# Performance work log

Measured on AMD Instinct MI355X. Metric: run time of the kernel, lower is better.

Reference implementation:

```python
import jax, jax.numpy as jnp
import numpy as np

LEN = 2048

def setup_inputs() -> dict:
    key = jax.random.key(0)
    k1, k2 = jax.random.split(key)
    x = jax.random.normal(k1, (LEN,), dtype=jnp.float32)
    y = jax.random.normal(k2, (LEN,), dtype=jnp.float32)
    return {"x": x, "y": y}

def reference(x, y):
    # Classic DTW DP with squared-difference cost.
    # Original torch code clamps indices with max(i-1,0)/max(j-1,0); because
    # DTW[i,j] is still +inf when read, the clamped reads reduce to the
    # standard recurrence: row 0 is a cumulative sum, col 0 uses only 'up',
    # interior uses min(up, left, diag).
    inf = jnp.float32(jnp.inf)
    cost0 = (x[0] - y) ** 2            # [len2]
    row0 = jnp.cumsum(cost0)           # DTW row i=0

    def row_step(prev_row, xi):
        cost = (xi - y) ** 2                                   # [len2]
        diag = jnp.concatenate([prev_row[:1], prev_row[:-1]])  # prev_row[j-1], clamped at j=0
        def cell(left, cud):
            c, up, dg = cud
            v = c + jnp.minimum(jnp.minimum(up, left), dg)
            return v, v
        # left init = inf => at j=0 min reduces to min(up, diag) = prev_row[0]
        _, new_row = jax.lax.scan(cell, inf, (cost, prev_row, diag))
        return new_row, None

    last_row, _ = jax.lax.scan(row_step, row0, x[1:])
    return jnp.sqrt(last_row[-1])
```

## Files before the change

### kernel.cpp

```cpp
#include <hip/hip_runtime.h>
#include <math.h>


#define NLEN   2048
#define NW     4
#define CSTEP  64
#define SPB    (CSTEP / 2)
#define DSKEW  192
#define PAD    128
#define RROW   (PAD + 2176)
#define YPAD   128
#define TAUMAX 2112
#define GTOT   (TAUMAX + (NW - 1) * DSKEW + CSTEP)
#define INFV   1e30f

typedef float f32x2 __attribute__((ext_vector_type(2)));

__device__ __forceinline__ float dpp_shr1(float v, float inj) {
    int r = __builtin_amdgcn_update_dpp(
        __builtin_bit_cast(int, inj), __builtin_bit_cast(int, v),
        0x138 , 0xF, 0xF, false );
    return __builtin_bit_cast(float, r);
}
__device__ __forceinline__ float rdlane(float v, int l) {
    return __builtin_bit_cast(float,
        __builtin_amdgcn_readlane(__builtin_bit_cast(int, v), l));
}
__device__ __forceinline__ float min3f(float a, float b, float c) {
    unsigned ia = __builtin_bit_cast(unsigned, a);
    unsigned ib = __builtin_bit_cast(unsigned, b);
    unsigned ic = __builtin_bit_cast(unsigned, c);
    unsigned m  = __builtin_elementwise_min(
                      __builtin_elementwise_min(ia, ib), ic);
    return __builtin_bit_cast(float, m);
}

__global__ __launch_bounds__(256, 1) void dtw_kernel(const float* __restrict__ X,
                                                     const float* __restrict__ Y,
                                                     float* __restrict__ out) {
    __shared__ __align__(16) float yB[YPAD + NLEN + YPAD];
    __shared__ float ring[(NW + 1) * RROW];
    float* yS = yB + YPAD;

    const int tid  = threadIdx.x;
    const int w    = tid >> 6;
    const int lane = tid & 63;

    {
        const float4* Y4 = (const float4*)Y;
        float4* y4 = (float4*)(yB + YPAD);
        y4[tid]       = Y4[tid];
        y4[tid + 256] = Y4[tid + 256];
        if (tid < YPAD) {
            yB[tid]               = INFV;
            yB[YPAD + NLEN + tid] = INFV;
        }
    }
    for (int k = tid; k < (NW + 1) * RROW; k += 256) ring[k] = INFV;
    __syncthreads();

    f32x2 xx0, xx1, xx2, xx3, xx4, xx5, xx6, xx7;
    {
        const float4 xa = *(const float4*)&X[tid * 8];
        const float4 xb = *(const float4*)&X[tid * 8 + 4];
        xx0 = (f32x2){xa.x, xa.x}; xx1 = (f32x2){xa.y, xa.y};
        xx2 = (f32x2){xa.z, xa.z}; xx3 = (f32x2){xa.w, xa.w};
        xx4 = (f32x2){xb.x, xb.x}; xx5 = (f32x2){xb.y, xb.y};
        xx6 = (f32x2){xb.z, xb.z}; xx7 = (f32x2){xb.w, xb.w};
    }

    float pB0 = INFV, pB1 = INFV, pB2 = INFV, pB3 = INFV;
    float pB4 = INFV, pB5 = INFV, pB6 = INFV, pB7 = INFV;
    float a7p = INFV;
    float uBp = (tid == 0) ? 0.0f : INFV;

    const float* ringR = ring + w * RROW + PAD;
    float*       ringW = ring + (w + 1) * RROW + PAD;

    for (int gb = 0; gb < GTOT; gb += CSTEP) {
        const int tau0 = gb - w * DSKEW;

        if (tau0 >= 0 && tau0 <= TAUMAX) {
            const float rblk = ringR[tau0 + lane];
            f32x2 y2[SPB];
            {
                const f32x2* yp = (const f32x2*)(yS + (tau0 - 2 * lane));
                #pragma unroll
                for (int k = 0; k < SPB; ++k) y2[k] = yp[k];
            }
            float* wp = ringW + (tau0 - 2 * lane);
            const bool isout = (tau0 == TAUMAX) & (w == NW - 1) & (lane == 63);

            #pragma unroll
            for (int s = 0; s < SPB; ++s) {
                const float riA = rdlane(rblk, 2 * s);
                const float riB = rdlane(rblk, 2 * s + 1);
                const float uA  = dpp_shr1(a7p, riA);
                const float uB  = dpp_shr1(pB7, riB);
                const f32x2 yv = y2[s];
                f32x2 d0 = xx0 - yv;
                float n0A = fmaf(d0.x, d0.x, min3f(pB0, uA,  uBp));
                float n0B = fmaf(d0.y, d0.y, min3f(n0A, uB,  uA));
                f32x2 d1 = xx1 - yv;
                float n1A = fmaf(d1.x, d1.x, min3f(pB1, n0A, pB0));
                float n1B = fmaf(d1.y, d1.y, min3f(n1A, n0B, n0A));
                f32x2 d2 = xx2 - yv;
                float n2A = fmaf(d2.x, d2.x, min3f(pB2, n1A, pB1));
                float n2B = fmaf(d2.y, d2.y, min3f(n2A, n1B, n1A));
                f32x2 d3 = xx3 - yv;
                float n3A = fmaf(d3.x, d3.x, min3f(pB3, n2A, pB2));
                float n3B = fmaf(d3.y, d3.y, min3f(n3A, n2B, n2A));
                f32x2 d4 = xx4 - yv;
                float n4A = fmaf(d4.x, d4.x, min3f(pB4, n3A, pB3));
                float n4B = fmaf(d4.y, d4.y, min3f(n4A, n3B, n3A));
                f32x2 d5 = xx5 - yv;
                float n5A = fmaf(d5.x, d5.x, min3f(pB5, n4A, pB4));
                float n5B = fmaf(d5.y, d5.y, min3f(n5A, n4B, n4A));
                f32x2 d6 = xx6 - yv;
                float n6A = fmaf(d6.x, d6.x, min3f(pB6, n5A, pB5));
                float n6B = fmaf(d6.y, d6.y, min3f(n6A, n5B, n5A));
                f32x2 d7 = xx7 - yv;
                float n7A = fmaf(d7.x, d7.x, min3f(pB7, n6A, pB6));
                float n7B = fmaf(d7.y, d7.y, min3f(n7A, n6B, n6A));
                f32x2 wv; wv.x = n7A; wv.y = n7B;
                *(f32x2*)(wp + 2 * s) = wv;
                uBp = uB; a7p = n7A;
                pB0 = n0B; pB1 = n1B; pB2 = n2B; pB3 = n3B;
                pB4 = n4B; pB5 = n5B; pB6 = n6B; pB7 = n7B;
                if (s == 30 && isout) out[0] = sqrtf(n7B);
            }
        }
        __syncthreads();
    }
}

extern "C" void kernel_launch(void* const* d_in, const int* in_sizes, int n_in,
                              void* d_out, int out_size, void* d_ws, size_t ws_size,
                              hipStream_t stream) {
    const float* x = (const float*)d_in[0];
    const float* y = (const float*)d_in[1];
    (void)in_sizes; (void)n_in; (void)out_size; (void)d_ws; (void)ws_size;
    dtw_kernel<<<1, 256, 0, stream>>>(x, y, (float*)d_out);
}
```

Before: 181.2 us.

## Split DTW wavefront across two workgroups with global-memory flag handoff

```diff
diff --git a/kernel.cpp b/kernel.cpp
--- a/kernel.cpp
+++ b/kernel.cpp
@@ -3,18 +3,21 @@
 
 
 #define NLEN   2048
-#define NW     4
+#define NWL    4
 #define CSTEP  64
 #define SPB    (CSTEP / 2)
 #define DSKEW  192
+#define EXTRA  128
 #define PAD    128
 #define RROW   (PAD + 2176)
 #define YPAD   128
 #define TAUMAX 2112
-#define GTOT   (TAUMAX + (NW - 1) * DSKEW + CSTEP)
+#define GTOT   (TAUMAX + 7 * DSKEW + EXTRA + CSTEP)
+#define FLAG_FINAL (TAUMAX + CSTEP)
 #define INFV   1e30f
 
 typedef float f32x2 __attribute__((ext_vector_type(2)));
+typedef unsigned long long u64;
 
 __device__ __forceinline__ float dpp_shr1(float v, float inj) {
     int r = __builtin_amdgcn_update_dpp(
@@ -34,17 +37,34 @@
                       __builtin_elementwise_min(ia, ib), ic);
     return __builtin_bit_cast(float, m);
 }
+__device__ __forceinline__ void spinflag(int* flag, int target) {
+    while (__hip_atomic_load(flag, __ATOMIC_ACQUIRE,
+                             __HIP_MEMORY_SCOPE_AGENT) < target)
+        __builtin_amdgcn_s_sleep(2);
+}
+__device__ __forceinline__ float gload(const float* p) {
+    unsigned u = __hip_atomic_load((const unsigned*)p, __ATOMIC_RELAXED,
+                                   __HIP_MEMORY_SCOPE_AGENT);
+    return __builtin_bit_cast(float, u);
+}
 
 __global__ __launch_bounds__(256, 1) void dtw_kernel(const float* __restrict__ X,
                                                      const float* __restrict__ Y,
-                                                     float* __restrict__ out) {
+                                                     float* __restrict__ out,
+                                                     float* __restrict__ ws) {
+    int*   flag = (int*)ws;
+    float* grow = ws + 16 + PAD;
+
     __shared__ __align__(16) float yB[YPAD + NLEN + YPAD];
-    __shared__ float ring[(NW + 1) * RROW];
+    __shared__ float ring[(NWL + 1) * RROW];
     float* yS = yB + YPAD;
 
     const int tid  = threadIdx.x;
     const int w    = tid >> 6;
     const int lane = tid & 63;
+    const int b    = blockIdx.x;
+    const int skew = (4 * b + w) * DSKEW + (b ? EXTRA : 0);
+    const int role = (b == 0) ? (w == 3 ? 1 : 0) : (w == 0 ? 2 : (w == 3 ? 3 : 0));
 
     {
         const float4* Y4 = (const float4*)Y;
@@ -56,7 +76,125 @@
             yB[YPAD + NLEN + tid] = INFV;
         }
     }
-    for (int k = tid; k < (NW + 1) * RROW; k += 256) ring[k] = INFV;
+    for (int k = tid; k < (NWL + 1) * RROW; k += 256) ring[k] = INFV;
+    __syncthreads();
+
+    f32x2 xx0, xx1, xx2, xx3;
+    {
+        const float4 xa = *(const float4*)&X[b * 1024 + w * 256 + lane * 4];
+        xx0 = (f32x2){xa.x, xa.x}; xx1 = (f32x2){xa.y, xa.y};
+        xx2 = (f32x2){xa.z, xa.z}; xx3 = (f32x2){xa.w, xa.w};
+    }
+
+    float pB0 = INFV, pB1 = INFV, pB2 = INFV, pB3 = INFV;
+    float a3p = INFV;
+    float uBp = (b == 0 && tid == 0) ? 0.0f : INFV;
+    float gcur = INFV, gnext = INFV;
+
+    const float* ringR = ring + w * RROW + PAD;
+    float*       ringW = ring + (w + 1) * RROW + PAD;
+
+    for (int gb = 0; gb < GTOT; gb += CSTEP) {
+        const int tau0 = gb - skew;
+
+        if (tau0 >= 0 && tau0 <= TAUMAX) {
+            float rblk;
+            if (role == 2) {
+                if (tau0 == 0) {
+                    spinflag(flag, 192);
+                    gcur = gload(grow + lane);
+                }
+                const int nt = tau0 + CSTEP;
+                if (nt <= TAUMAX) {
+                    int tgt = nt + 192;
+                    if (tgt > FLAG_FINAL) tgt = FLAG_FINAL;
+                    spinflag(flag, tgt);
+                    gnext = gload(grow + nt + lane);
+                }
+                rblk = gcur;
+            } else {
+                rblk = ringR[tau0 + lane];
+            }
+
+            f32x2 y2[SPB];
+            {
+                const f32x2* yp = (const f32x2*)(yS + (tau0 - 2 * lane));
+                #pragma unroll
+                for (int k = 0; k < SPB; ++k) y2[k] = yp[k];
+            }
+            float* wp = ringW + (tau0 - 2 * lane);
+            u64*   gw = (u64*)(grow + (tau0 - 2 * lane));
+            const bool isout = (role == 3) & (lane == 63) & (tau0 == TAUMAX);
+
+            #pragma unroll
+            for (int s = 0; s < SPB; ++s) {
+                const float riA = rdlane(rblk, 2 * s);
+                const float riB = rdlane(rblk, 2 * s + 1);
+                const float uA  = dpp_shr1(a3p, riA);
+                const float uB  = dpp_shr1(pB3, riB);
+                const f32x2 yv = y2[s];
+                f32x2 d0 = xx0 - yv;
+                float n0A = fmaf(d0.x, d0.x, min3f(pB0, uA,  uBp));
+                float n0B = fmaf(d0.y, d0.y, min3f(n0A, uB,  uA));
+                f32x2 d1 = xx1 - yv;
+                float n1A = fmaf(d1.x, d1.x, min3f(pB1, n0A, pB0));
+                float n1B = fmaf(d1.y, d1.y, min3f(n1A, n0B, n0A));
+                f32x2 d2 = xx2 - yv;
+                float n2A = fmaf(d2.x, d2.x, min3f(pB2, n1A, pB1));
+                float n2B = fmaf(d2.y, d2.y, min3f(n2A, n1B, n1A));
+                f32x2 d3 = xx3 - yv;
+                float n3A = fmaf(d3.x, d3.x, min3f(pB3, n2A, pB2));
+                float n3B = fmaf(d3.y, d3.y, min3f(n3A, n2B, n2A));
+                f32x2 wv; wv.x = n3A; wv.y = n3B;
+                if (role == 1) {
+                    __hip_atomic_store(gw + s, __builtin_bit_cast(u64, wv),
+                                       __ATOMIC_RELAXED, __HIP_MEMORY_SCOPE_AGENT);
+                } else if (role != 3) {
+                    *(f32x2*)(wp + 2 * s) = wv;
+                }
+                uBp = uB; a3p = n3A;
+                pB0 = n0B; pB1 = n1B; pB2 = n2B; pB3 = n3B;
+                if (s == 30 && isout) out[0] = sqrtf(n3B);
+            }
+
+            if (role == 1) {
+                __threadfence();
+                if (lane == 0)
+                    __hip_atomic_store(flag, tau0 + CSTEP, __ATOMIC_RELEASE,
+                                       __HIP_MEMORY_SCOPE_AGENT);
+            }
+            if (role == 2) gcur = gnext;
+        }
+        __syncthreads();
+    }
+}
+
+#define FNW    4
+#define FDSKEW 192
+#define FGTOT  (TAUMAX + (FNW - 1) * FDSKEW + CSTEP)
+
+__global__ __launch_bounds__(256, 1) void dtw_kernel_fb(const float* __restrict__ X,
+                                                        const float* __restrict__ Y,
+                                                        float* __restrict__ out) {
+    __shared__ __align__(16) float yB[YPAD + NLEN + YPAD];
+    __shared__ float ring[(FNW + 1) * RROW];
+    float* yS = yB + YPAD;
+
+    const int tid  = threadIdx.x;
+    const int w    = tid >> 6;
+    const int lane = tid & 63;
+
+    {
+        const float4* Y4 = (const float4*)Y;
+        float4* y4 = (float4*)(yB + YPAD);
+        y4[tid]       = Y4[tid];
+        y4[tid + 256] = Y4[tid + 256];
+        if (tid < YPAD) {
+            yB[tid]               = INFV;
+            yB[YPAD + NLEN + tid] = INFV;
+        }
+    }
+    for (int k = tid; k < (FNW + 1) * RROW; k += 256) ring[k] = INFV;
     __syncthreads();
 
     f32x2 xx0, xx1, xx2, xx3, xx4, xx5, xx6, xx7;
@@ -77,8 +215,8 @@
     const float* ringR = ring + w * RROW + PAD;
     float*       ringW = ring + (w + 1) * RROW + PAD;
 
-    for (int gb = 0; gb < GTOT; gb += CSTEP) {
-        const int tau0 = gb - w * DSKEW;
+    for (int gb = 0; gb < FGTOT; gb += CSTEP) {
+        const int tau0 = gb - w * FDSKEW;
 
         if (tau0 >= 0 && tau0 <= TAUMAX) {
             const float rblk = ringR[tau0 + lane];
@@ -89,7 +227,7 @@
                 for (int k = 0; k < SPB; ++k) y2[k] = yp[k];
             }
             float* wp = ringW + (tau0 - 2 * lane);
-            const bool isout = (tau0 == TAUMAX) & (w == NW - 1) & (lane == 63);
+            const bool isout = (tau0 == TAUMAX) & (w == FNW - 1) & (lane == 63);
 
             #pragma unroll
             for (int s = 0; s < SPB; ++s) {
@@ -139,6 +277,11 @@
                               hipStream_t stream) {
     const float* x = (const float*)d_in[0];
     const float* y = (const float*)d_in[1];
-    (void)in_sizes; (void)n_in; (void)out_size; (void)d_ws; (void)ws_size;
-    dtw_kernel<<<1, 256, 0, stream>>>(x, y, (float*)d_out);
-}
+    (void)in_sizes; (void)n_in; (void)out_size;
+    if (d_ws != nullptr && ws_size >= 16384) {
+        hipMemsetAsync(d_ws, 0, 4, stream);
+        dtw_kernel<<<2, 256, 0, stream>>>(x, y, (float*)d_out, (float*)d_ws);
+    } else {
+        dtw_kernel_fb<<<1, 256, 0, stream>>>(x, y, (float*)d_out);
+    }
+}
```

Measured after the change: 268.6 us. 48.2% more time.

## Split DTW wavefront across 8 waves with 4 rows per thread

Applied to the files above, without the earlier changes.

```diff
diff --git a/kernel.cpp b/kernel.cpp
--- a/kernel.cpp
+++ b/kernel.cpp
@@ -3,14 +3,14 @@
 
 
 #define NLEN   2048
-#define NW     4
-#define CSTEP  64
+#define NW     8
+#define CSTEP  32
 #define SPB    (CSTEP / 2)
-#define DSKEW  192
+#define DSKEW  160
 #define PAD    128
 #define RROW   (PAD + 2176)
 #define YPAD   128
-#define TAUMAX 2112
+#define TAUMAX 2144
 #define GTOT   (TAUMAX + (NW - 1) * DSKEW + CSTEP)
 #define INFV   1e30f
 
@@ -35,7 +35,7 @@
     return __builtin_bit_cast(float, m);
 }
 
-__global__ __launch_bounds__(256, 1) void dtw_kernel(const float* __restrict__ X,
+__global__ __launch_bounds__(512, 1) void dtw_kernel(const float* __restrict__ X,
                                                      const float* __restrict__ Y,
                                                      float* __restrict__ out) {
     __shared__ __align__(16) float yB[YPAD + NLEN + YPAD];
@@ -49,29 +49,24 @@
     {
         const float4* Y4 = (const float4*)Y;
         float4* y4 = (float4*)(yB + YPAD);
-        y4[tid]       = Y4[tid];
-        y4[tid + 256] = Y4[tid + 256];
+        y4[tid] = Y4[tid];
         if (tid < YPAD) {
             yB[tid]               = INFV;
             yB[YPAD + NLEN + tid] = INFV;
         }
     }
-    for (int k = tid; k < (NW + 1) * RROW; k += 256) ring[k] = INFV;
+    for (int k = tid; k < (NW + 1) * RROW; k += 512) ring[k] = INFV;
     __syncthreads();
 
-    f32x2 xx0, xx1, xx2, xx3, xx4, xx5, xx6, xx7;
+    f32x2 xx0, xx1, xx2, xx3;
     {
-        const float4 xa = *(const float4*)&X[tid * 8];
-        const float4 xb = *(const float4*)&X[tid * 8 + 4];
+        const float4 xa = *(const float4*)&X[tid * 4];
         xx0 = (f32x2){xa.x, xa.x}; xx1 = (f32x2){xa.y, xa.y};
         xx2 = (f32x2){xa.z, xa.z}; xx3 = (f32x2){xa.w, xa.w};
-        xx4 = (f32x2){xb.x, xb.x}; xx5 = (f32x2){xb.y, xb.y};
-        xx6 = (f32x2){xb.z, xb.z}; xx7 = (f32x2){xb.w, xb.w};
     }
 
     float pB0 = INFV, pB1 = INFV, pB2 = INFV, pB3 = INFV;
-    float pB4 = INFV, pB5 = INFV, pB6 = INFV, pB7 = INFV;
-    float a7p = INFV;
+    float a3p = INFV;
     float uBp = (tid == 0) ? 0.0f : INFV;
 
     const float* ringR = ring + w * RROW + PAD;
@@ -95,8 +90,8 @@
             for (int s = 0; s < SPB; ++s) {
                 const float riA = rdlane(rblk, 2 * s);
                 const float riB = rdlane(rblk, 2 * s + 1);
-                const float uA  = dpp_shr1(a7p, riA);
-                const float uB  = dpp_shr1(pB7, riB);
+                const float uA  = dpp_shr1(a3p, riA);
+                const float uB  = dpp_shr1(pB3, riB);
                 const f32x2 yv = y2[s];
                 f32x2 d0 = xx0 - yv;
                 float n0A = fmaf(d0.x, d0.x, min3f(pB0, uA,  uBp));
@@ -110,24 +105,11 @@
                 f32x2 d3 = xx3 - yv;
                 float n3A = fmaf(d3.x, d3.x, min3f(pB3, n2A, pB2));
                 float n3B = fmaf(d3.y, d3.y, min3f(n3A, n2B, n2A));
-                f32x2 d4 = xx4 - yv;
-                float n4A = fmaf(d4.x, d4.x, min3f(pB4, n3A, pB3));
-                float n4B = fmaf(d4.y, d4.y, min3f(n4A, n3B, n3A));
-                f32x2 d5 = xx5 - yv;
-                float n5A = fmaf(d5.x, d5.x, min3f(pB5, n4A, pB4));
-                float n5B = fmaf(d5.y, d5.y, min3f(n5A, n4B, n4A));
-                f32x2 d6 = xx6 - yv;
-                float n6A = fmaf(d6.x, d6.x, min3f(pB6, n5A, pB5));
-                float n6B = fmaf(d6.y, d6.y, min3f(n6A, n5B, n5A));
-                f32x2 d7 = xx7 - yv;
-                float n7A = fmaf(d7.x, d7.x, min3f(pB7, n6A, pB6));
-                float n7B = fmaf(d7.y, d7.y, min3f(n7A, n6B, n6A));
-                f32x2 wv; wv.x = n7A; wv.y = n7B;
+                f32x2 wv; wv.x = n3A; wv.y = n3B;
                 *(f32x2*)(wp + 2 * s) = wv;
-                uBp = uB; a7p = n7A;
+                uBp = uB; a3p = n3A;
                 pB0 = n0B; pB1 = n1B; pB2 = n2B; pB3 = n3B;
-                pB4 = n4B; pB5 = n5B; pB6 = n6B; pB7 = n7B;
-                if (s == 30 && isout) out[0] = sqrtf(n7B);
+                if (s == 14 && isout) out[0] = sqrtf(n3B);
             }
         }
         __syncthreads();
@@ -140,5 +122,5 @@
     const float* x = (const float*)d_in[0];
     const float* y = (const float*)d_in[1];
     (void)in_sizes; (void)n_in; (void)out_size; (void)d_ws; (void)ws_size;
-    dtw_kernel<<<1, 256, 0, stream>>>(x, y, (float*)d_out);
+    dtw_kernel<<<1, 512, 0, stream>>>(x, y, (float*)d_out);
 }
```

After: 198.1 us. 1.09x slower.
